# Optimization experiments

Hardware: AMD Instinct MI355X
Metric: run time of the kernel (lower is better)

Reference implementation:

```python
import jax, jax.numpy as jnp
import numpy as np
from math import sqrt

SIZE = 4096
NR_CORES = 2
RANK = 16
D = 64  # core_size: D**NR_CORES == SIZE


def setup_inputs() -> dict:
    key = jax.random.key(0)
    k_x, k_c0, k_c1, k_b = jax.random.split(key, 4)
    t = 1.0 / sqrt(SIZE)
    sigma = (t * sqrt(RANK) ** (1 - NR_CORES)) ** (1.0 / NR_CORES)
    x = jax.random.normal(k_x, (2, 4096, SIZE), dtype=jnp.float32)
    core0 = sigma * jax.random.normal(k_c0, (D, D, D, RANK, 1), dtype=jnp.float32)
    core1 = sigma * jax.random.normal(k_c1, (D, D, D, 1, RANK), dtype=jnp.float32)
    bias = sqrt(1.0 / SIZE) * jax.random.uniform(k_b, (SIZE,), minval=-1.0, maxval=1.0, dtype=jnp.float32)
    return {"x": x, "core0": core0, "core1": core1, "bias": bias}


def _btt_forward(x, cores, bias):
    d, c, size = D, NR_CORES, SIZE
    G = cores[0]  # (d,...,d, r, 1)
    for idx, core in enumerate(cores[1:]):
        j = d ** (idx + 1)
        i = d ** (c - idx - 1)
        core_r = core.reshape(j, d, i, core.shape[-2], core.shape[-1])
        G_r = G.reshape(j, d ** (idx + 1), i, G.shape[-2], G.shape[-1])
        # contract rank dim b: (j,x,i,cb) x (j,y,i,ba) -> (j,x,y,i,c,a)
        G = jnp.einsum('jxicb,jyiba->jxyica', core_r, G_r)
    G = G.reshape(size, size)
    out = x.reshape(-1, size) @ G + bias
    return out.reshape(x.shape)


def reference(x, core0, core1, bias):
    return _btt_forward(x, [core0, core1], bias)
```

## Files before the change

kernel.cpp:

```cpp
#include <hip/hip_runtime.h>
#include <hip/hip_bf16.h>
#include <stdint.h>
#include <stddef.h>

using bf16 = __hip_bfloat16;

typedef __attribute__((ext_vector_type(4))) float f32x4;
typedef __attribute__((ext_vector_type(8))) short bf16x8;
typedef __attribute__((ext_vector_type(4))) unsigned short u16x4;

#define K_DIM 4096
#define M_ROWS 8192
#define BM 256
#define BN 256
#define BK 64
#define NT (K_DIM / BK)
#define MT2 (M_ROWS / BM)
#define NT2 (K_DIM / BN)

template<int M> struct MC { static constexpr int value = M; };

__global__ void conv_bf16(const float* __restrict__ in, bf16* __restrict__ outb, int n4) {
  int idx = blockIdx.x * blockDim.x + threadIdx.x;
  int stride = gridDim.x * blockDim.x;
  for (int k = idx; k < n4; k += stride) {
    f32x4 v = ((const f32x4*)in)[k];
    bf16 tmp[4];
    tmp[0] = __float2bfloat16(v.x);
    tmp[1] = __float2bfloat16(v.y);
    tmp[2] = __float2bfloat16(v.z);
    tmp[3] = __float2bfloat16(v.w);
    ((u16x4*)outb)[k] = *(const u16x4*)tmp;
  }
}

__global__ void build_gt(const float* __restrict__ core0, const float* __restrict__ core1,
                         bf16* __restrict__ GT) {
  int j = blockIdx.x >> 6;
  int i = blockIdx.x & 63;
  __shared__ float c0s[64][16];
  __shared__ float c1s[64][16];
  int t = threadIdx.x;
#pragma unroll
  for (int rep = 0; rep < 4; ++rep) {
    int idx = rep * 256 + t;
    int row = idx >> 4;
    int b = idx & 15;
    size_t base = ((size_t)(j * 64 + row) * 64 + i) * 16 + b;
    c1s[row][b] = core1[base];
    c0s[row][b] = core0[base];
  }
  __syncthreads();
  int x = t & 63;
  int ys = t >> 6;
  float r1[16];
#pragma unroll
  for (int b = 0; b < 16; ++b) r1[b] = c1s[x][b];
#pragma unroll
  for (int yy = 0; yy < 16; ++yy) {
    int y = ys * 16 + yy;
    float acc = 0.f;
#pragma unroll
    for (int b = 0; b < 16; ++b) acc += r1[b] * c0s[y][b];
    GT[((size_t)(y * 64 + i) << 12) + (size_t)(j * 64 + x)] = __float2bfloat16(acc);
  }
}

__device__ __forceinline__ void gload_lds16(const bf16* g, bf16* l) {
  __builtin_amdgcn_global_load_lds(
      (const __attribute__((address_space(1))) unsigned int*)(g),
      (__attribute__((address_space(3))) unsigned int*)(l),
      16, 0, 0);
}

template<int MH>
__device__ __forceinline__ void read_a(bf16x8 (&af)[4][2], const bf16* As,
                                       int abase, int swk0, int swk1) {
#pragma unroll
  for (int mi = 0; mi < 4; ++mi) {
    int off = abase + (MH * 4 + mi) * 1024;
    af[mi][0] = *(const bf16x8*)&As[off + swk0];
    af[mi][1] = *(const bf16x8*)&As[off + swk1];
  }
}

template<int NH>
__device__ __forceinline__ void read_b(bf16x8 (&bfr)[4][2], const bf16* Bs,
                                       int bbase, int swk0, int swk1) {
#pragma unroll
  for (int ni = 0; ni < 2; ++ni) {
    int off = bbase + (NH * 2 + ni) * 1024;
    bfr[NH * 2 + ni][0] = *(const bf16x8*)&Bs[off + swk0];
    bfr[NH * 2 + ni][1] = *(const bf16x8*)&Bs[off + swk1];
  }
}

template<int MH, int NH>
__device__ __forceinline__ void mfma_quad(f32x4 (&acc)[8][4], const bf16x8 (&af)[4][2],
                                          const bf16x8 (&bfr)[4][2]) {
#pragma unroll
  for (int mi = 0; mi < 4; ++mi)
#pragma unroll
    for (int ni = 0; ni < 2; ++ni)
#pragma unroll
      for (int kk = 0; kk < 2; ++kk)
        acc[MH * 4 + mi][NH * 2 + ni] = __builtin_amdgcn_mfma_f32_16x16x32_bf16(
            af[mi][kk], bfr[NH * 2 + ni][kk], acc[MH * 4 + mi][NH * 2 + ni], 0, 0, 0);
}

#define BARRIER() __builtin_amdgcn_s_barrier()
#define SP1() __builtin_amdgcn_s_setprio(1)
#define SP0() __builtin_amdgcn_s_setprio(0)
#define VMCNT4() asm volatile("s_waitcnt vmcnt(4)" ::: "memory")
#define VMCNT0() asm volatile("s_waitcnt vmcnt(0)" ::: "memory")

__global__ __launch_bounds__(512, 2)
void gemm_xg(const bf16* __restrict__ Xb, const bf16* __restrict__ GT,
             const float* __restrict__ bias, float* __restrict__ out) {
  __shared__ bf16 As[2][BM * BK];
  __shared__ bf16 Bs[2][BN * BK];

  int bid = blockIdx.x;
  int sb = (bid & 7) * (MT2 * NT2 / 8) + (bid >> 3);
  int bm = sb >> 4;
  int bn = sb & 15;

  int t = threadIdx.x;
  int lane = t & 63;
  int wid = t >> 6;

  int srow = t >> 3;
  int scol = t & 7;
  int sxor = scol ^ (srow & 7);
  const bf16* gA0 = Xb + ((size_t)(bm * BM + srow) * K_DIM) + sxor * 8;
  const bf16* gB0 = GT + ((size_t)(bn * BN + srow) * K_DIM) + sxor * 8;
  int lbase = srow * BK + scol * 8;

  auto sA = [&](int buf, int h, int kt) {
    const bf16* g = gA0 + (size_t)(h * 128) * K_DIM + (size_t)kt * BK;
    bf16* l = &As[buf][h * 128 * BK + lbase];
    gload_lds16(g, l);
    gload_lds16(g + (size_t)64 * K_DIM, l + 64 * BK);
  };
  auto sB = [&](int buf, int h, int kt) {
    const bf16* g = gB0 + (size_t)(h * 128) * K_DIM + (size_t)kt * BK;
    bf16* l = &Bs[buf][h * 128 * BK + lbase];
    gload_lds16(g, l);
    gload_lds16(g + (size_t)64 * K_DIM, l + 64 * BK);
  };

  int wm = wid >> 2;
  int wn = wid & 3;
  int lr = lane & 15;
  int g4 = lane >> 4;
  int x7 = lr & 7;
  int swk0 = ((g4 ^ x7) << 3);
  int swk1 = (((4 + g4) ^ x7) << 3);
  int abase = (wm * 128 + lr) * BK;
  int bbase = (wn * 64 + lr) * BK;

  f32x4 acc[8][4] = {};
  bf16x8 af[4][2];
  bf16x8 bfr[4][2];

  auto tile = [&](int kt, const bf16* Ab, const bf16* Bb, int obuf, int cbuf, auto mode) {
    constexpr int MODE = decltype(mode)::value;
    if (MODE == 2) { VMCNT0(); } else { VMCNT4(); }
    BARRIER();
    if (MODE < 2) { sA(obuf, 0, kt + 1); sA(obuf, 1, kt + 1); }
    read_a<0>(af, Ab, abase, swk0, swk1);
    read_b<0>(bfr, Bb, bbase, swk0, swk1);
    read_b<1>(bfr, Bb, bbase, swk0, swk1);
    SP1();
    mfma_quad<0, 0>(acc, af, bfr);
    mfma_quad<0, 1>(acc, af, bfr);
    SP0();
    read_a<1>(af, Ab, abase, swk0, swk1);
    SP1();
    mfma_quad<1, 0>(acc, af, bfr);
    mfma_quad<1, 1>(acc, af, bfr);
    SP0();
    BARRIER();
    if (MODE == 0) { sB(cbuf, 0, kt + 2); sB(cbuf, 1, kt + 2); }
  };

  const bf16* A0 = &As[0][0];
  const bf16* B0 = &Bs[0][0];
  const bf16* A1 = &As[1][0];
  const bf16* B1 = &Bs[1][0];

  sB(0, 0, 0); sB(0, 1, 0);
  sA(0, 0, 0); sA(0, 1, 0);
  sB(1, 0, 1); sB(1, 1, 1);

#pragma unroll 1
  for (int i = 0; i < NT / 2 - 1; ++i) {
    tile(2 * i,     A0, B0, 1, 0, MC<0>{});
    tile(2 * i + 1, A1, B1, 0, 1, MC<0>{});
  }
  tile(NT - 2, A0, B0, 1, 0, MC<1>{});
  tile(NT - 1, A1, B1, 0, 1, MC<2>{});

  int colbase = bn * BN + wn * 64 + lr;
  int rowbase = bm * BM + wm * 128 + g4 * 4;
#pragma unroll
  for (int ni = 0; ni < 4; ++ni) {
    int col = colbase + ni * 16;
    float bv = bias[col];
#pragma unroll
    for (int mi = 0; mi < 8; ++mi) {
#pragma unroll
      for (int r = 0; r < 4; ++r) {
        int row = rowbase + mi * 16 + r;
        out[(size_t)row * K_DIM + col] = acc[mi][ni][r] + bv;
      }
    }
  }
}

extern "C" void kernel_launch(void* const* d_in, const int* in_sizes, int n_in,
                              void* d_out, int out_size, void* d_ws, size_t ws_size,
                              hipStream_t stream) {
  const float* x     = (const float*)d_in[0];
  const float* core0 = (const float*)d_in[1];
  const float* core1 = (const float*)d_in[2];
  const float* bias  = (const float*)d_in[3];
  float* out = (float*)d_out;

  bf16* Xb = (bf16*)d_ws;
  bf16* GT = (bf16*)((char*)d_ws + (size_t)M_ROWS * K_DIM * sizeof(bf16));

  conv_bf16<<<2048, 256, 0, stream>>>(x, Xb, (M_ROWS * K_DIM) / 4);
  build_gt<<<4096, 256, 0, stream>>>(core0, core1, GT);
  gemm_xg<<<MT2 * NT2, 512, 0, stream>>>(Xb, GT, bias, out);
}
```

Measured before the change: 297.4 us.

## Restructure GEMM main loop into software-pipelined schedule with interleaved loads and MFMAs

```diff
diff --git a/kernel.cpp b/kernel.cpp
--- a/kernel.cpp
+++ b/kernel.cpp
@@ -108,11 +108,13 @@
             af[mi][kk], bfr[NH * 2 + ni][kk], acc[MH * 4 + mi][NH * 2 + ni], 0, 0, 0);
 }
 
-#define BARRIER() __builtin_amdgcn_s_barrier()
+#define BARRIER() asm volatile("s_barrier" ::: "memory")
 #define SP1() __builtin_amdgcn_s_setprio(1)
 #define SP0() __builtin_amdgcn_s_setprio(0)
+#define VMCNT8() asm volatile("s_waitcnt vmcnt(8)" ::: "memory")
 #define VMCNT4() asm volatile("s_waitcnt vmcnt(4)" ::: "memory")
 #define VMCNT0() asm volatile("s_waitcnt vmcnt(0)" ::: "memory")
+#define LGKM0()  asm volatile("s_waitcnt lgkmcnt(0)" ::: "memory")
 
 __global__ __launch_bounds__(512, 2)
 void gemm_xg(const bf16* __restrict__ Xb, const bf16* __restrict__ GT,
@@ -163,43 +165,57 @@
   bf16x8 af[4][2];
   bf16x8 bfr[4][2];
 
-  auto tile = [&](int kt, const bf16* Ab, const bf16* Bb, int obuf, int cbuf, auto mode) {
-    constexpr int MODE = decltype(mode)::value;
-    if (MODE == 2) { VMCNT0(); } else { VMCNT4(); }
-    BARRIER();
-    if (MODE < 2) { sA(obuf, 0, kt + 1); sA(obuf, 1, kt + 1); }
-    read_a<0>(af, Ab, abase, swk0, swk1);
-    read_b<0>(bfr, Bb, bbase, swk0, swk1);
-    read_b<1>(bfr, Bb, bbase, swk0, swk1);
-    SP1();
-    mfma_quad<0, 0>(acc, af, bfr);
-    mfma_quad<0, 1>(acc, af, bfr);
-    SP0();
-    read_a<1>(af, Ab, abase, swk0, swk1);
-    SP1();
-    mfma_quad<1, 0>(acc, af, bfr);
-    mfma_quad<1, 1>(acc, af, bfr);
-    SP0();
-    BARRIER();
-    if (MODE == 0) { sB(cbuf, 0, kt + 2); sB(cbuf, 1, kt + 2); }
-  };
-
-  const bf16* A0 = &As[0][0];
-  const bf16* B0 = &Bs[0][0];
-  const bf16* A1 = &As[1][0];
-  const bf16* B1 = &Bs[1][0];
+  const bf16* Ab[2] = { &As[0][0], &As[1][0] };
+  const bf16* Bb[2] = { &Bs[0][0], &Bs[1][0] };
 
   sB(0, 0, 0); sB(0, 1, 0);
   sA(0, 0, 0); sA(0, 1, 0);
   sB(1, 0, 1); sB(1, 1, 1);
+  sA(1, 0, 1); sA(1, 1, 1);
+  VMCNT8();
+  BARRIER();
+  read_a<0>(af, Ab[0], abase, swk0, swk1);
+  read_b<0>(bfr, Bb[0], bbase, swk0, swk1);
+  read_b<1>(bfr, Bb[0], bbase, swk0, swk1);
+  LGKM0();
+  BARRIER();
+
+  auto tile = [&](int kt, int CUR, auto modec) {
+    constexpr int MODE = decltype(modec)::value;
+    const int OTH = CUR ^ 1;
+    const bf16* Ac = Ab[CUR];
+    const bf16* Ao = Ab[OTH];
+    const bf16* Bo = Bb[OTH];
+
+    SP1(); mfma_quad<0, 0>(acc, af, bfr); SP0();
+    if (MODE == 0) sB(CUR, 0, kt + 2);
+    SP1(); mfma_quad<0, 1>(acc, af, bfr); SP0();
+    read_a<1>(af, Ac, abase, swk0, swk1);
+    if (MODE == 0) sB(CUR, 1, kt + 2);
+    LGKM0();
+    if (MODE == 0) { VMCNT4(); } else { VMCNT0(); }
+    BARRIER();
+
+    SP1(); mfma_quad<1, 0>(acc, af, bfr); SP0();
+    if (MODE < 2) read_b<0>(bfr, Bo, bbase, swk0, swk1);
+    if (MODE == 0) sA(CUR, 0, kt + 2);
+    SP1(); mfma_quad<1, 1>(acc, af, bfr); SP0();
+    if (MODE < 2) {
+      read_b<1>(bfr, Bo, bbase, swk0, swk1);
+      read_a<0>(af, Ao, abase, swk0, swk1);
+    }
+    if (MODE == 0) sA(CUR, 1, kt + 2);
+    LGKM0();
+    BARRIER();
+  };
 
 #pragma unroll 1
   for (int i = 0; i < NT / 2 - 1; ++i) {
-    tile(2 * i,     A0, B0, 1, 0, MC<0>{});
-    tile(2 * i + 1, A1, B1, 0, 1, MC<0>{});
-  }
-  tile(NT - 2, A0, B0, 1, 0, MC<1>{});
-  tile(NT - 1, A1, B1, 0, 1, MC<2>{});
+    tile(2 * i,     0, MC<0>{});
+    tile(2 * i + 1, 1, MC<0>{});
+  }
+  tile(NT - 2, 0, MC<1>{});
+  tile(NT - 1, 1, MC<2>{});
 
   int colbase = bn * BN + wn * 64 + lr;
   int rowbase = bm * BM + wm * 128 + g4 * 4;
```

Result: no change. 295.4 us (-0.7%).

## Switch GEMM to 32x32x16 MFMA with register double-buffered LDS reads

Applied to the files above, without the earlier changes.

```diff
diff --git a/kernel.cpp b/kernel.cpp
--- a/kernel.cpp
+++ b/kernel.cpp
@@ -6,6 +6,7 @@
 using bf16 = __hip_bfloat16;
 
 typedef __attribute__((ext_vector_type(4))) float f32x4;
+typedef __attribute__((ext_vector_type(16))) float f32x16;
 typedef __attribute__((ext_vector_type(8))) short bf16x8;
 typedef __attribute__((ext_vector_type(4))) unsigned short u16x4;
 
@@ -18,7 +19,7 @@
 #define MT2 (M_ROWS / BM)
 #define NT2 (K_DIM / BN)
 
-template<int M> struct MC { static constexpr int value = M; };
+template<bool B> struct BC { static constexpr bool value = B; };
 
 __global__ void conv_bf16(const float* __restrict__ in, bf16* __restrict__ outb, int n4) {
   int idx = blockIdx.x * blockDim.x + threadIdx.x;
@@ -73,45 +74,9 @@
       16, 0, 0);
 }
 
-template<int MH>
-__device__ __forceinline__ void read_a(bf16x8 (&af)[4][2], const bf16* As,
-                                       int abase, int swk0, int swk1) {
-#pragma unroll
-  for (int mi = 0; mi < 4; ++mi) {
-    int off = abase + (MH * 4 + mi) * 1024;
-    af[mi][0] = *(const bf16x8*)&As[off + swk0];
-    af[mi][1] = *(const bf16x8*)&As[off + swk1];
-  }
-}
-
-template<int NH>
-__device__ __forceinline__ void read_b(bf16x8 (&bfr)[4][2], const bf16* Bs,
-                                       int bbase, int swk0, int swk1) {
-#pragma unroll
-  for (int ni = 0; ni < 2; ++ni) {
-    int off = bbase + (NH * 2 + ni) * 1024;
-    bfr[NH * 2 + ni][0] = *(const bf16x8*)&Bs[off + swk0];
-    bfr[NH * 2 + ni][1] = *(const bf16x8*)&Bs[off + swk1];
-  }
-}
-
-template<int MH, int NH>
-__device__ __forceinline__ void mfma_quad(f32x4 (&acc)[8][4], const bf16x8 (&af)[4][2],
-                                          const bf16x8 (&bfr)[4][2]) {
-#pragma unroll
-  for (int mi = 0; mi < 4; ++mi)
-#pragma unroll
-    for (int ni = 0; ni < 2; ++ni)
-#pragma unroll
-      for (int kk = 0; kk < 2; ++kk)
-        acc[MH * 4 + mi][NH * 2 + ni] = __builtin_amdgcn_mfma_f32_16x16x32_bf16(
-            af[mi][kk], bfr[NH * 2 + ni][kk], acc[MH * 4 + mi][NH * 2 + ni], 0, 0, 0);
-}
-
 #define BARRIER() __builtin_amdgcn_s_barrier()
 #define SP1() __builtin_amdgcn_s_setprio(1)
 #define SP0() __builtin_amdgcn_s_setprio(0)
-#define VMCNT4() asm volatile("s_waitcnt vmcnt(4)" ::: "memory")
 #define VMCNT0() asm volatile("s_waitcnt vmcnt(0)" ::: "memory")
 
 __global__ __launch_bounds__(512, 2)
@@ -151,37 +116,37 @@
 
   int wm = wid >> 2;
   int wn = wid & 3;
-  int lr = lane & 15;
-  int g4 = lane >> 4;
-  int x7 = lr & 7;
-  int swk0 = ((g4 ^ x7) << 3);
-  int swk1 = (((4 + g4) ^ x7) << 3);
-  int abase = (wm * 128 + lr) * BK;
-  int bbase = (wn * 64 + lr) * BK;
-
-  f32x4 acc[8][4] = {};
-  bf16x8 af[4][2];
-  bf16x8 bfr[4][2];
-
-  auto tile = [&](int kt, const bf16* Ab, const bf16* Bb, int obuf, int cbuf, auto mode) {
-    constexpr int MODE = decltype(mode)::value;
-    if (MODE == 2) { VMCNT0(); } else { VMCNT4(); }
-    BARRIER();
-    if (MODE < 2) { sA(obuf, 0, kt + 1); sA(obuf, 1, kt + 1); }
-    read_a<0>(af, Ab, abase, swk0, swk1);
-    read_b<0>(bfr, Bb, bbase, swk0, swk1);
-    read_b<1>(bfr, Bb, bbase, swk0, swk1);
+  int l31 = lane & 31;
+  int lh = lane >> 5;
+  int x7 = l31 & 7;
+  int abase = (wm * 128 + l31) * BK;
+  int bbase = (wn * 64 + l31) * BK;
+  int so[4];
+#pragma unroll
+  for (int s = 0; s < 4; ++s) so[s] = (((2 * s + lh) ^ x7) << 3);
+
+  f32x16 acc[4][2] = {};
+  bf16x8 a0[4], b0[2], a1[4], b1[2];
+
+  auto readset = [&](bf16x8 (&af)[4], bf16x8 (&bv)[2],
+                     const bf16* Ab, const bf16* Bb, int s) {
+    int sofs = so[s];
+#pragma unroll
+    for (int mi = 0; mi < 4; ++mi)
+      af[mi] = *(const bf16x8*)&Ab[abase + mi * 2048 + sofs];
+#pragma unroll
+    for (int ni = 0; ni < 2; ++ni)
+      bv[ni] = *(const bf16x8*)&Bb[bbase + ni * 2048 + sofs];
+  };
+  auto mstep = [&](bf16x8 (&af)[4], bf16x8 (&bv)[2]) {
     SP1();
-    mfma_quad<0, 0>(acc, af, bfr);
-    mfma_quad<0, 1>(acc, af, bfr);
+#pragma unroll
+    for (int mi = 0; mi < 4; ++mi)
+#pragma unroll
+      for (int ni = 0; ni < 2; ++ni)
+        acc[mi][ni] = __builtin_amdgcn_mfma_f32_32x32x16_bf16(
+            af[mi], bv[ni], acc[mi][ni], 0, 0, 0);
     SP0();
-    read_a<1>(af, Ab, abase, swk0, swk1);
-    SP1();
-    mfma_quad<1, 0>(acc, af, bfr);
-    mfma_quad<1, 1>(acc, af, bfr);
-    SP0();
-    BARRIER();
-    if (MODE == 0) { sB(cbuf, 0, kt + 2); sB(cbuf, 1, kt + 2); }
   };
 
   const bf16* A0 = &As[0][0];
@@ -189,29 +154,49 @@
   const bf16* A1 = &As[1][0];
   const bf16* B1 = &Bs[1][0];
 
+  auto tile = [&](int kt, const bf16* Ac, const bf16* Bc, int obuf, auto lastc) {
+    constexpr bool LAST = decltype(lastc)::value;
+    if (!LAST) { sA(obuf, 0, kt + 1); sA(obuf, 1, kt + 1); }
+    readset(a1, b1, Ac, Bc, 1);
+    mstep(a0, b0);
+    if (!LAST) { sB(obuf, 0, kt + 1); sB(obuf, 1, kt + 1); }
+    readset(a0, b0, Ac, Bc, 2);
+    mstep(a1, b1);
+    readset(a1, b1, Ac, Bc, 3);
+    mstep(a0, b0);
+    VMCNT0();
+    mstep(a1, b1);
+    BARRIER();
+  };
+
+  sA(0, 0, 0); sA(0, 1, 0);
   sB(0, 0, 0); sB(0, 1, 0);
-  sA(0, 0, 0); sA(0, 1, 0);
-  sB(1, 0, 1); sB(1, 1, 1);
+  VMCNT0();
+  BARRIER();
+  readset(a0, b0, A0, B0, 0);
 
 #pragma unroll 1
   for (int i = 0; i < NT / 2 - 1; ++i) {
-    tile(2 * i,     A0, B0, 1, 0, MC<0>{});
-    tile(2 * i + 1, A1, B1, 0, 1, MC<0>{});
-  }
-  tile(NT - 2, A0, B0, 1, 0, MC<1>{});
-  tile(NT - 1, A1, B1, 0, 1, MC<2>{});
-
-  int colbase = bn * BN + wn * 64 + lr;
-  int rowbase = bm * BM + wm * 128 + g4 * 4;
-#pragma unroll
-  for (int ni = 0; ni < 4; ++ni) {
-    int col = colbase + ni * 16;
+    tile(2 * i, A0, B0, 1, BC<false>{});
+    readset(a0, b0, A1, B1, 0);
+    tile(2 * i + 1, A1, B1, 0, BC<false>{});
+    readset(a0, b0, A0, B0, 0);
+  }
+  tile(NT - 2, A0, B0, 1, BC<false>{});
+  readset(a0, b0, A1, B1, 0);
+  tile(NT - 1, A1, B1, 0, BC<true>{});
+
+  int colbase = bn * BN + wn * 64 + l31;
+  int rowbase = bm * BM + wm * 128 + 4 * lh;
+#pragma unroll
+  for (int ni = 0; ni < 2; ++ni) {
+    int col = colbase + ni * 32;
     float bv = bias[col];
 #pragma unroll
-    for (int mi = 0; mi < 8; ++mi) {
-#pragma unroll
-      for (int r = 0; r < 4; ++r) {
-        int row = rowbase + mi * 16 + r;
+    for (int mi = 0; mi < 4; ++mi) {
+#pragma unroll
+      for (int r = 0; r < 16; ++r) {
+        int row = rowbase + mi * 32 + (r & 3) + 8 * (r >> 2);
         out[(size_t)row * K_DIM + col] = acc[mi][ni][r] + bv;
       }
     }
```

New measurement: 310.5 us. 4.4% more time.

## Restructure GEMM main loop into four barrier-separated phases with next-tile LDS prefetch

Applied to the files above, without the earlier changes.

```diff
diff --git a/kernel.cpp b/kernel.cpp
--- a/kernel.cpp
+++ b/kernel.cpp
@@ -73,12 +73,11 @@
       16, 0, 0);
 }
 
-template<int MH>
-__device__ __forceinline__ void read_a(bf16x8 (&af)[4][2], const bf16* As,
-                                       int abase, int swk0, int swk1) {
+__device__ __forceinline__ void read_ah(bf16x8 (&af)[4][2], const bf16* As,
+                                        int abaseMH, int swk0, int swk1) {
 #pragma unroll
   for (int mi = 0; mi < 4; ++mi) {
-    int off = abase + (MH * 4 + mi) * 1024;
+    int off = abaseMH + mi * 1024;
     af[mi][0] = *(const bf16x8*)&As[off + swk0];
     af[mi][1] = *(const bf16x8*)&As[off + swk1];
   }
@@ -160,29 +159,9 @@
   int bbase = (wn * 64 + lr) * BK;
 
   f32x4 acc[8][4] = {};
-  bf16x8 af[4][2];
+  bf16x8 af0[4][2];
+  bf16x8 af1[4][2];
   bf16x8 bfr[4][2];
-
-  auto tile = [&](int kt, const bf16* Ab, const bf16* Bb, int obuf, int cbuf, auto mode) {
-    constexpr int MODE = decltype(mode)::value;
-    if (MODE == 2) { VMCNT0(); } else { VMCNT4(); }
-    BARRIER();
-    if (MODE < 2) { sA(obuf, 0, kt + 1); sA(obuf, 1, kt + 1); }
-    read_a<0>(af, Ab, abase, swk0, swk1);
-    read_b<0>(bfr, Bb, bbase, swk0, swk1);
-    read_b<1>(bfr, Bb, bbase, swk0, swk1);
-    SP1();
-    mfma_quad<0, 0>(acc, af, bfr);
-    mfma_quad<0, 1>(acc, af, bfr);
-    SP0();
-    read_a<1>(af, Ab, abase, swk0, swk1);
-    SP1();
-    mfma_quad<1, 0>(acc, af, bfr);
-    mfma_quad<1, 1>(acc, af, bfr);
-    SP0();
-    BARRIER();
-    if (MODE == 0) { sB(cbuf, 0, kt + 2); sB(cbuf, 1, kt + 2); }
-  };
 
   const bf16* A0 = &As[0][0];
   const bf16* B0 = &Bs[0][0];
@@ -192,14 +171,44 @@
   sB(0, 0, 0); sB(0, 1, 0);
   sA(0, 0, 0); sA(0, 1, 0);
   sB(1, 0, 1); sB(1, 1, 1);
+  VMCNT4();
+  BARRIER();
+  read_ah(af0, A0, abase, swk0, swk1);
+  read_b<0>(bfr, B0, bbase, swk0, swk1);
+
+  auto tile = [&](int kt, const bf16* Ac, const bf16* Bc,
+                  const bf16* Ao, const bf16* Bo,
+                  int bufAn, int bufBn, auto modec) {
+    constexpr int MODE = decltype(modec)::value;
+
+    read_b<1>(bfr, Bc, bbase, swk0, swk1);
+    if (MODE < 2) sA(bufAn, 0, kt + 1);
+    BARRIER(); SP1(); mfma_quad<0, 0>(acc, af0, bfr); SP0(); BARRIER();
+
+    read_ah(af1, Ac, abase + 4096, swk0, swk1);
+    if (MODE < 2) sA(bufAn, 1, kt + 1);
+    BARRIER(); SP1(); mfma_quad<0, 1>(acc, af0, bfr); SP0(); BARRIER();
+
+    if (MODE == 0) sB(bufBn, 0, kt + 2);
+    BARRIER(); SP1(); mfma_quad<1, 0>(acc, af1, bfr); SP0(); BARRIER();
+
+    if (MODE == 0) sB(bufBn, 1, kt + 2);
+    if (MODE == 0) { VMCNT4(); } else if (MODE == 1) { VMCNT0(); }
+    BARRIER();
+    if (MODE < 2) {
+      read_ah(af0, Ao, abase, swk0, swk1);
+      read_b<0>(bfr, Bo, bbase, swk0, swk1);
+    }
+    SP1(); mfma_quad<1, 1>(acc, af1, bfr); SP0(); BARRIER();
+  };
 
 #pragma unroll 1
   for (int i = 0; i < NT / 2 - 1; ++i) {
-    tile(2 * i,     A0, B0, 1, 0, MC<0>{});
-    tile(2 * i + 1, A1, B1, 0, 1, MC<0>{});
-  }
-  tile(NT - 2, A0, B0, 1, 0, MC<1>{});
-  tile(NT - 1, A1, B1, 0, 1, MC<2>{});
+    tile(2 * i,     A0, B0, A1, B1, 1, 0, MC<0>{});
+    tile(2 * i + 1, A1, B1, A0, B0, 0, 1, MC<0>{});
+  }
+  tile(NT - 2, A0, B0, A1, B1, 1, 0, MC<1>{});
+  tile(NT - 1, A1, B1, A0, B0, 0, 1, MC<2>{});
 
   int colbase = bn * BN + wn * 64 + lr;
   int rowbase = bm * BM + wm * 128 + g4 * 4;
```

Measured after the change: 318.5 us. 7.1% more time.
